# Optimization experiments

Measured on AMD Instinct MI355X. Metric: run time of the kernel, lower is better.

## Reference

```python
import jax, jax.numpy as jnp
import numpy as np

N, FIN, H, FOUT = 4096, 128, 4, 64
NEG_INF = -1e9


def _xavier(key, shape):
    fan_in, fan_out = shape[-2], shape[-1]
    limit = float(np.sqrt(6.0 / (fan_in + fan_out)))
    return jax.random.uniform(key, shape, jnp.float32, -limit, limit)


def setup_inputs() -> dict:
    key = jax.random.key(0)
    ks = jax.random.split(key, 7)
    x = jax.random.normal(ks[0], (N, FIN), jnp.float32)
    u = jax.random.uniform(ks[1], (N, N))
    mask = jnp.where(u < 0.02, 0.0, NEG_INF).astype(jnp.float32)
    idx = jnp.arange(N)
    mask = mask.at[idx, idx].set(0.0)
    proj_param = _xavier(ks[2], (H, FIN, FOUT))          # per-head projection
    score_src = _xavier(ks[3], (H, FOUT, 1))             # scoring_fn_source (IMP1 layout)
    score_tgt = _xavier(ks[4], (H, FOUT, 1))             # scoring_fn_target
    skip_w = _xavier(ks[5], (H * FOUT, FIN))             # skip_proj Linear weight
    bias = jnp.zeros((H * FOUT,), jnp.float32)
    return {"x": x, "mask": mask, "proj_param": proj_param,
            "score_src": score_src, "score_tgt": score_tgt,
            "skip_w": skip_w, "bias": bias}


def reference(x, mask, proj_param, score_src, score_tgt, skip_w, bias):
    # project: [1,N,Fin] @ [H,Fin,Fout] -> [H,N,Fout]
    h = jnp.einsum('nf,hfo->hno', x, proj_param)
    # additive (Bahdanau-style) scores
    s_src = jnp.matmul(h, score_src)                     # [H,N,1]
    s_tgt = jnp.matmul(h, score_tgt)                     # [H,N,1]
    all_scores = jax.nn.leaky_relu(s_src + jnp.swapaxes(s_tgt, 1, 2), 0.2)  # [H,N,N]
    attn = jax.nn.softmax(all_scores + mask[None, :, :], axis=-1)           # [H,N,N]
    # aggregate: [H,N,N] @ [H,N,Fout] -> [N,H,Fout]
    out = jnp.einsum('hnm,hmo->nho', attn, h)
    # skip connection (dims differ: Fin != H*Fout -> use skip_proj)
    out = out + jnp.matmul(x, skip_w.T).reshape(N, H, FOUT)
    out = out.reshape(N, H * FOUT) + bias                # concat heads + bias
    return jax.nn.elu(out)
```

## Files before the change

### kernel.cpp

```cpp
#include <hip/hip_runtime.h>
#include <hip/hip_bf16.h>
#include <math.h>


#define NN   4096
#define FIN  128
#define NH   4
#define FO   64
#define HF   256
#define SEG  96
#define LIST 192
#define GEMM_BLOCKS 512
#define SCAN_BLOCKS 1024
#define ROWS_PER    4

typedef unsigned short ushort_t;
typedef unsigned int uint4n __attribute__((ext_vector_type(4)));

__device__ __forceinline__ ushort_t f2bf(float f) {
    __hip_bfloat16 h = __float2bfloat16(f);
    union { __hip_bfloat16 h; ushort_t u; } c; c.h = h; return c.u;
}
__device__ __forceinline__ float bf2f(ushort_t u) {
    union { unsigned int i; float f; } c; c.i = ((unsigned int)u) << 16; return c.f;
}

__global__ __launch_bounds__(256) void k0_fused(
        const float* __restrict__ x,
        const float* __restrict__ proj,
        const float* __restrict__ skw,
        const float* __restrict__ asrc,
        const float* __restrict__ atgt,
        const unsigned int* __restrict__ mask,
        ushort_t* __restrict__ h2b, float* __restrict__ skip_ws,
        float* __restrict__ src4, float* __restrict__ tgt4,
        ushort_t* __restrict__ list, int* __restrict__ cnt) {
    __shared__ float sA[64 * 68];
    __shared__ float sB[64 * 64];
    const int tid = threadIdx.x;
    const int blk = blockIdx.x;

    if (blk >= GEMM_BLOCKS) {
        ushort_t* s_nbr = (ushort_t*)sA;
        int (*s_wt)[4]  = (int(*)[4])sB;
        const int lane = tid & 63, w = tid >> 6;
        const int row0 = (blk - GEMM_BLOCKS) * ROWS_PER;
        const uint4n* mb = (const uint4n*)mask;
        const size_t wl = (size_t)(w * 256 + lane);

        uint4n cur[4], nxt[4];
        #pragma unroll
        for (int s = 0; s < 4; s++)
            cur[s] = mb[(size_t)row0 * 1024 + wl + s * 64];

        for (int rr = 0; rr < ROWS_PER; rr++) {
            const int i = row0 + rr;
            if (rr + 1 < ROWS_PER) {
                #pragma unroll
                for (int s = 0; s < 4; s++)
                    nxt[s] = mb[(size_t)(i + 1) * 1024 + wl + s * 64];
            }
            int base = 0;
            #pragma unroll
            for (int s = 0; s < 4; s++) {
                #pragma unroll
                for (int e = 0; e < 4; e++) {
                    bool hit = (cur[s][e] & 0x7fffffffu) == 0u;
                    unsigned long long bal = __ballot(hit);
                    int pre = __builtin_amdgcn_mbcnt_hi(
                                  (unsigned int)(bal >> 32),
                                  __builtin_amdgcn_mbcnt_lo((unsigned int)bal, 0));
                    if (hit) {
                        int slot = base + pre;
                        if (slot < SEG)
                            s_nbr[w * SEG + slot] =
                                (ushort_t)(w * 1024 + s * 256 + lane * 4 + e);
                    }
                    base += (int)__popcll(bal);
                }
            }
            const int p = rr & 1;
            if (lane == 0) s_wt[p][w] = base < SEG ? base : SEG;
            __syncthreads();
            const int t0 = s_wt[p][0], t1 = s_wt[p][1],
                      t2 = s_wt[p][2], t3 = s_wt[p][3];
            const int off = (w > 0 ? t0 : 0) + (w > 1 ? t1 : 0) + (w > 2 ? t2 : 0);
            const int mine = s_wt[p][w];
            ushort_t* dst = list + (size_t)i * LIST;
            for (int kk = lane; kk < mine; kk += 64) {
                int pp = off + kk;
                if (pp < LIST) dst[pp] = s_nbr[w * SEG + kk];
            }
            if (tid == 0) {
                int tot = t0 + t1 + t2 + t3;
                cnt[i] = tot < LIST ? tot : LIST;
            }
            #pragma unroll
            for (int s = 0; s < 4; s++) cur[s] = nxt[s];
        }
        return;
    }

    const int bc = blk >> 6;
    const int i0 = (blk & 63) * 64;
    const int tx = tid & 15, ty = tid >> 4;
    const int r0 = ty << 2, c0 = tx << 2;
    float acc[4][4] = {};

    #pragma unroll
    for (int kb = 0; kb < FIN; kb += 64) {
        if (kb) __syncthreads();
        #pragma unroll
        for (int q = 0; q < 4; q++) {
            int s   = tid + q * 256;
            int row = s >> 4;
            int c4  = (s & 15) << 2;
            float4 v = *(const float4*)(x + (size_t)(i0 + row) * FIN + kb + c4);
            float* d = sA + row * 68 + c4;
            d[0] = v.x; d[1] = v.y; d[2] = v.z; d[3] = v.w;
        }
        if (bc < 4) {
            const float4* src = (const float4*)(proj + (size_t)bc * FIN * FO
                                                + (size_t)kb * FO);
            #pragma unroll
            for (int q = 0; q < 4; q++) {
                int s = tid + q * 256;
                *(float4*)(sB + (size_t)s * 4) = src[s];
            }
        } else {
            const float* sw = skw + (size_t)(bc - 4) * 64 * FIN;
            #pragma unroll
            for (int q = 0; q < 4; q++) {
                int s  = tid + q * 256;
                int c  = s & 63;
                int k4 = (s >> 6) << 2;
                float4 v = *(const float4*)(sw + (size_t)c * FIN + kb + k4);
                sB[(k4 + 0) * 64 + c] = v.x;
                sB[(k4 + 1) * 64 + c] = v.y;
                sB[(k4 + 2) * 64 + c] = v.z;
                sB[(k4 + 3) * 64 + c] = v.w;
            }
        }
        __syncthreads();

        #pragma unroll 2
        for (int k = 0; k < 64; k += 4) {
            alignas(16) float a[4][4];
            alignas(16) float b[4][4];
            #pragma unroll
            for (int rr = 0; rr < 4; rr++)
                *(float4*)a[rr] = *(const float4*)(sA + (r0 + rr) * 68 + k);
            #pragma unroll
            for (int kk = 0; kk < 4; kk++)
                *(float4*)b[kk] = *(const float4*)(sB + (k + kk) * 64 + c0);
            #pragma unroll
            for (int kk = 0; kk < 4; kk++)
                #pragma unroll
                for (int rr = 0; rr < 4; rr++)
                    #pragma unroll
                    for (int cc = 0; cc < 4; cc++)
                        acc[rr][cc] = fmaf(a[rr][kk], b[kk][cc], acc[rr][cc]);
        }
    }

    if (bc < 4) {
        #pragma unroll
        for (int rr = 0; rr < 4; rr++) {
            ushort4 hv;
            hv.x = f2bf(acc[rr][0]); hv.y = f2bf(acc[rr][1]);
            hv.z = f2bf(acc[rr][2]); hv.w = f2bf(acc[rr][3]);
            *(ushort4*)(h2b + (size_t)(i0 + r0 + rr) * HF + bc * 64 + c0) = hv;
        }
        float as[4], at[4];
        #pragma unroll
        for (int cc = 0; cc < 4; cc++) {
            as[cc] = asrc[bc * FO + c0 + cc];
            at[cc] = atgt[bc * FO + c0 + cc];
        }
        #pragma unroll
        for (int rr = 0; rr < 4; rr++) {
            float ps = acc[rr][0] * as[0] + acc[rr][1] * as[1]
                     + acc[rr][2] * as[2] + acc[rr][3] * as[3];
            float pt = acc[rr][0] * at[0] + acc[rr][1] * at[1]
                     + acc[rr][2] * at[2] + acc[rr][3] * at[3];
            #pragma unroll
            for (int off = 8; off >= 1; off >>= 1) {
                ps += __shfl_xor(ps, off, 64);
                pt += __shfl_xor(pt, off, 64);
            }
            if (tx == 0) {
                int i = i0 + r0 + rr;
                src4[(size_t)i * 4 + bc] = ps;
                tgt4[(size_t)i * 4 + bc] = pt;
            }
        }
    } else {
        float* dst = skip_ws + (size_t)i0 * HF + (bc - 4) * 64;
        #pragma unroll
        for (int rr = 0; rr < 4; rr++)
            *(float4*)(dst + (size_t)(r0 + rr) * HF + c0) = *(float4*)acc[rr];
    }
}

__global__ __launch_bounds__(256) void k2b_attn(
        const ushort_t* __restrict__ list,
        const int* __restrict__ cnt,
        const ushort_t* __restrict__ h2b,
        const float* __restrict__ skip_ws,
        const float* __restrict__ src4,
        const float* __restrict__ tgt4,
        const float* __restrict__ bias,
        float* __restrict__ out) {
    __shared__ float s_p[4][LIST];
    __shared__ int   s_j[LIST];
    const int tid  = threadIdx.x;
    const int lane = tid & 63, w = tid >> 6;
    const int i    = blockIdx.x;
    const int col  = w * 64 + lane;

    const float skipv = skip_ws[(size_t)i * HF + col];
    const float bv    = bias[col];
    const float sc    = src4[(size_t)i * 4 + w];
    int c = cnt[i];
    c = c < LIST ? c : LIST;

    const ushort_t* lp = list + (size_t)i * LIST;
    for (int kk = tid; kk < c; kk += 256) s_j[kk] = lp[kk];
    __syncthreads();

    float lsum = 0.f;
    for (int kk = lane; kk < c; kk += 64) {
        int j = s_j[kk];
        float p = sc + tgt4[(size_t)j * 4 + w];
        p = p > 0.f ? p : 0.2f * p;
        p = __expf(p);
        s_p[w][kk] = p;
        lsum += p;
    }
    #pragma unroll
    for (int off = 32; off >= 1; off >>= 1)
        lsum += __shfl_xor(lsum, off, 64);
    const float inv = lsum > 0.f ? 1.0f / lsum : 0.0f;

    const ushort_t* hp = h2b + col;
    const float* ps = s_p[w];
    float acc = 0.f;
    int kk = 0;
    for (; kk + 8 <= c; kk += 8) {
        int j0 = s_j[kk + 0], j1 = s_j[kk + 1], j2 = s_j[kk + 2], j3 = s_j[kk + 3];
        int j4 = s_j[kk + 4], j5 = s_j[kk + 5], j6 = s_j[kk + 6], j7 = s_j[kk + 7];
        float p0 = ps[kk + 0], p1 = ps[kk + 1], p2 = ps[kk + 2], p3 = ps[kk + 3];
        float p4 = ps[kk + 4], p5 = ps[kk + 5], p6 = ps[kk + 6], p7 = ps[kk + 7];
        float h0 = bf2f(hp[(size_t)j0 * HF]);
        float h1 = bf2f(hp[(size_t)j1 * HF]);
        float h2v = bf2f(hp[(size_t)j2 * HF]);
        float h3 = bf2f(hp[(size_t)j3 * HF]);
        float h4 = bf2f(hp[(size_t)j4 * HF]);
        float h5 = bf2f(hp[(size_t)j5 * HF]);
        float h6 = bf2f(hp[(size_t)j6 * HF]);
        float h7 = bf2f(hp[(size_t)j7 * HF]);
        acc = fmaf(p0, h0, acc);  acc = fmaf(p1, h1, acc);
        acc = fmaf(p2, h2v, acc); acc = fmaf(p3, h3, acc);
        acc = fmaf(p4, h4, acc);  acc = fmaf(p5, h5, acc);
        acc = fmaf(p6, h6, acc);  acc = fmaf(p7, h7, acc);
    }
    for (; kk < c; kk++)
        acc = fmaf(ps[kk], bf2f(hp[(size_t)s_j[kk] * HF]), acc);

    float vv = acc * inv + skipv + bv;
    vv = vv > 0.f ? vv : expm1f(vv);
    out[(size_t)i * HF + col] = vv;
}

extern "C" void kernel_launch(void* const* d_in, const int* in_sizes, int n_in,
                              void* d_out, int out_size, void* d_ws, size_t ws_size,
                              hipStream_t stream) {
    const float*        x    = (const float*)d_in[0];
    const unsigned int* mask = (const unsigned int*)d_in[1];
    const float*        proj = (const float*)d_in[2];
    const float*        asrc = (const float*)d_in[3];
    const float*        atgt = (const float*)d_in[4];
    const float*        skw  = (const float*)d_in[5];
    const float*        bias = (const float*)d_in[6];
    float*              out  = (float*)d_out;

    char* ws = (char*)d_ws;
    ushort_t* h2b     = (ushort_t*)ws;
    float*    skip_ws = (float*)(ws + (2u << 20));
    float*    src4    = (float*)(ws + (6u << 20));
    float*    tgt4    = (float*)(ws + (6u << 20) + (64u << 10));
    ushort_t* list    = (ushort_t*)(ws + (8u << 20));
    int*      cntp    = (int*)(ws + (10u << 20));

    hipLaunchKernelGGL(k0_fused, dim3(GEMM_BLOCKS + SCAN_BLOCKS), dim3(256),
                       0, stream,
                       x, proj, skw, asrc, atgt, mask,
                       h2b, skip_ws, src4, tgt4, list, cntp);
    hipLaunchKernelGGL(k2b_attn, dim3(NN), dim3(256), 0, stream,
                       list, cntp, h2b, skip_ws, src4, tgt4, bias, out);
}
```

Baseline: 135.9 us.

## Fuse mask scan into attention kernel and vectorize neighbor gather by row

The mask-to-neighbor-list compaction moves out of the GEMM kernel and into the attention kernel. Each block now scans its own mask row into shared memory, so the list and count no longer go through global memory. The aggregation now has each wave take every fourth neighbor and load a full 256-wide bf16 row as ushort4 per lane, with the four wave partials reduced through shared memory. The cost is that the mask read (64 MB) now sits on the attention kernel's critical path instead of overlapping with the GEMM blocks, plus extra syncs and shared-memory use per block.

New measurement: 127.1 us. 6.5% less time.

```diff
diff --git a/kernel.cpp b/kernel.cpp
--- a/kernel.cpp
+++ b/kernel.cpp
@@ -11,8 +11,6 @@
 #define SEG  96
 #define LIST 192
 #define GEMM_BLOCKS 512
-#define SCAN_BLOCKS 1024
-#define ROWS_PER    4
 
 typedef unsigned short ushort_t;
 typedef unsigned int uint4n __attribute__((ext_vector_type(4)));
@@ -25,81 +23,18 @@
     union { unsigned int i; float f; } c; c.i = ((unsigned int)u) << 16; return c.f;
 }
 
-__global__ __launch_bounds__(256) void k0_fused(
+__global__ __launch_bounds__(256) void k0_gemm(
         const float* __restrict__ x,
         const float* __restrict__ proj,
         const float* __restrict__ skw,
         const float* __restrict__ asrc,
         const float* __restrict__ atgt,
-        const unsigned int* __restrict__ mask,
         ushort_t* __restrict__ h2b, float* __restrict__ skip_ws,
-        float* __restrict__ src4, float* __restrict__ tgt4,
-        ushort_t* __restrict__ list, int* __restrict__ cnt) {
+        float* __restrict__ src4, float* __restrict__ tgt4) {
     __shared__ float sA[64 * 68];
     __shared__ float sB[64 * 64];
     const int tid = threadIdx.x;
     const int blk = blockIdx.x;
-
-    if (blk >= GEMM_BLOCKS) {
-        ushort_t* s_nbr = (ushort_t*)sA;
-        int (*s_wt)[4]  = (int(*)[4])sB;
-        const int lane = tid & 63, w = tid >> 6;
-        const int row0 = (blk - GEMM_BLOCKS) * ROWS_PER;
-        const uint4n* mb = (const uint4n*)mask;
-        const size_t wl = (size_t)(w * 256 + lane);
-
-        uint4n cur[4], nxt[4];
-        #pragma unroll
-        for (int s = 0; s < 4; s++)
-            cur[s] = mb[(size_t)row0 * 1024 + wl + s * 64];
-
-        for (int rr = 0; rr < ROWS_PER; rr++) {
-            const int i = row0 + rr;
-            if (rr + 1 < ROWS_PER) {
-                #pragma unroll
-                for (int s = 0; s < 4; s++)
-                    nxt[s] = mb[(size_t)(i + 1) * 1024 + wl + s * 64];
-            }
-            int base = 0;
-            #pragma unroll
-            for (int s = 0; s < 4; s++) {
-                #pragma unroll
-                for (int e = 0; e < 4; e++) {
-                    bool hit = (cur[s][e] & 0x7fffffffu) == 0u;
-                    unsigned long long bal = __ballot(hit);
-                    int pre = __builtin_amdgcn_mbcnt_hi(
-                                  (unsigned int)(bal >> 32),
-                                  __builtin_amdgcn_mbcnt_lo((unsigned int)bal, 0));
-                    if (hit) {
-                        int slot = base + pre;
-                        if (slot < SEG)
-                            s_nbr[w * SEG + slot] =
-                                (ushort_t)(w * 1024 + s * 256 + lane * 4 + e);
-                    }
-                    base += (int)__popcll(bal);
-                }
-            }
-            const int p = rr & 1;
-            if (lane == 0) s_wt[p][w] = base < SEG ? base : SEG;
-            __syncthreads();
-            const int t0 = s_wt[p][0], t1 = s_wt[p][1],
-                      t2 = s_wt[p][2], t3 = s_wt[p][3];
-            const int off = (w > 0 ? t0 : 0) + (w > 1 ? t1 : 0) + (w > 2 ? t2 : 0);
-            const int mine = s_wt[p][w];
-            ushort_t* dst = list + (size_t)i * LIST;
-            for (int kk = lane; kk < mine; kk += 64) {
-                int pp = off + kk;
-                if (pp < LIST) dst[pp] = s_nbr[w * SEG + kk];
-            }
-            if (tid == 0) {
-                int tot = t0 + t1 + t2 + t3;
-                cnt[i] = tot < LIST ? tot : LIST;
-            }
-            #pragma unroll
-            for (int s = 0; s < 4; s++) cur[s] = nxt[s];
-        }
-        return;
-    }
 
     const int bc = blk >> 6;
     const int i0 = (blk & 63) * 64;
@@ -202,30 +137,66 @@
     }
 }
 
-__global__ __launch_bounds__(256) void k2b_attn(
-        const ushort_t* __restrict__ list,
-        const int* __restrict__ cnt,
+__global__ __launch_bounds__(256) void k1_attn(
+        const unsigned int* __restrict__ mask,
         const ushort_t* __restrict__ h2b,
         const float* __restrict__ skip_ws,
         const float* __restrict__ src4,
         const float* __restrict__ tgt4,
         const float* __restrict__ bias,
         float* __restrict__ out) {
-    __shared__ float s_p[4][LIST];
-    __shared__ int   s_j[LIST];
+    __shared__ ushort_t s_seg[4][SEG];
+    __shared__ int      s_j[LIST];
+    __shared__ float    s_p[4][LIST + 1];
+    __shared__ float    s_red[4][256];
+    __shared__ int      s_cnt[4];
+    __shared__ float    s_inv[4];
+
     const int tid  = threadIdx.x;
     const int lane = tid & 63, w = tid >> 6;
     const int i    = blockIdx.x;
-    const int col  = w * 64 + lane;
-
-    const float skipv = skip_ws[(size_t)i * HF + col];
-    const float bv    = bias[col];
+
+    const uint4n* mb = (const uint4n*)mask + (size_t)i * 1024;
+    uint4n cur[4];
+    #pragma unroll
+    for (int s = 0; s < 4; s++)
+        cur[s] = mb[w * 256 + lane + s * 64];
+
+    const float skipv = skip_ws[(size_t)i * HF + tid];
+    const float bv    = bias[tid];
     const float sc    = src4[(size_t)i * 4 + w];
-    int c = cnt[i];
+
+    int base = 0;
+    #pragma unroll
+    for (int s = 0; s < 4; s++) {
+        #pragma unroll
+        for (int e = 0; e < 4; e++) {
+            bool hit = (cur[s][e] & 0x7fffffffu) == 0u;
+            unsigned long long bal = __ballot(hit);
+            int pre = __builtin_amdgcn_mbcnt_hi(
+                          (unsigned int)(bal >> 32),
+                          __builtin_amdgcn_mbcnt_lo((unsigned int)bal, 0));
+            if (hit) {
+                int slot = base + pre;
+                if (slot < SEG)
+                    s_seg[w][slot] =
+                        (ushort_t)(w * 1024 + s * 256 + lane * 4 + e);
+            }
+            base += (int)__popcll(bal);
+        }
+    }
+    if (lane == 0) s_cnt[w] = base < SEG ? base : SEG;
+    __syncthreads();
+
+    const int t0 = s_cnt[0], t1 = s_cnt[1], t2 = s_cnt[2], t3 = s_cnt[3];
+    const int off  = (w > 0 ? t0 : 0) + (w > 1 ? t1 : 0) + (w > 2 ? t2 : 0);
+    const int mine = s_cnt[w];
+    for (int kk = lane; kk < mine; kk += 64) {
+        int pp = off + kk;
+        if (pp < LIST) s_j[pp] = s_seg[w][kk];
+    }
+    int c = t0 + t1 + t2 + t3;
     c = c < LIST ? c : LIST;
-
-    const ushort_t* lp = list + (size_t)i * LIST;
-    for (int kk = tid; kk < c; kk += 256) s_j[kk] = lp[kk];
     __syncthreads();
 
     float lsum = 0.f;
@@ -238,38 +209,45 @@
         lsum += p;
     }
     #pragma unroll
-    for (int off = 32; off >= 1; off >>= 1)
-        lsum += __shfl_xor(lsum, off, 64);
-    const float inv = lsum > 0.f ? 1.0f / lsum : 0.0f;
-
-    const ushort_t* hp = h2b + col;
-    const float* ps = s_p[w];
-    float acc = 0.f;
-    int kk = 0;
-    for (; kk + 8 <= c; kk += 8) {
-        int j0 = s_j[kk + 0], j1 = s_j[kk + 1], j2 = s_j[kk + 2], j3 = s_j[kk + 3];
-        int j4 = s_j[kk + 4], j5 = s_j[kk + 5], j6 = s_j[kk + 6], j7 = s_j[kk + 7];
-        float p0 = ps[kk + 0], p1 = ps[kk + 1], p2 = ps[kk + 2], p3 = ps[kk + 3];
-        float p4 = ps[kk + 4], p5 = ps[kk + 5], p6 = ps[kk + 6], p7 = ps[kk + 7];
-        float h0 = bf2f(hp[(size_t)j0 * HF]);
-        float h1 = bf2f(hp[(size_t)j1 * HF]);
-        float h2v = bf2f(hp[(size_t)j2 * HF]);
-        float h3 = bf2f(hp[(size_t)j3 * HF]);
-        float h4 = bf2f(hp[(size_t)j4 * HF]);
-        float h5 = bf2f(hp[(size_t)j5 * HF]);
-        float h6 = bf2f(hp[(size_t)j6 * HF]);
-        float h7 = bf2f(hp[(size_t)j7 * HF]);
-        acc = fmaf(p0, h0, acc);  acc = fmaf(p1, h1, acc);
-        acc = fmaf(p2, h2v, acc); acc = fmaf(p3, h3, acc);
-        acc = fmaf(p4, h4, acc);  acc = fmaf(p5, h5, acc);
-        acc = fmaf(p6, h6, acc);  acc = fmaf(p7, h7, acc);
-    }
-    for (; kk < c; kk++)
-        acc = fmaf(ps[kk], bf2f(hp[(size_t)s_j[kk] * HF]), acc);
-
-    float vv = acc * inv + skipv + bv;
+    for (int o = 32; o >= 1; o >>= 1)
+        lsum += __shfl_xor(lsum, o, 64);
+    if (lane == 0) s_inv[w] = lsum > 0.f ? 1.0f / lsum : 0.0f;
+    __syncthreads();
+
+    const int h = lane >> 4;
+    const ushort_t* hp = h2b + 4 * lane;
+    float4 acc = {0.f, 0.f, 0.f, 0.f};
+    int kk = w;
+    for (; kk + 4 < c; kk += 8) {
+        int   j0 = s_j[kk],        j1 = s_j[kk + 4];
+        float p0 = s_p[h][kk],     p1 = s_p[h][kk + 4];
+        ushort4 a0 = *(const ushort4*)(hp + (size_t)j0 * HF);
+        ushort4 a1 = *(const ushort4*)(hp + (size_t)j1 * HF);
+        acc.x = fmaf(p0, bf2f(a0.x), acc.x);
+        acc.y = fmaf(p0, bf2f(a0.y), acc.y);
+        acc.z = fmaf(p0, bf2f(a0.z), acc.z);
+        acc.w = fmaf(p0, bf2f(a0.w), acc.w);
+        acc.x = fmaf(p1, bf2f(a1.x), acc.x);
+        acc.y = fmaf(p1, bf2f(a1.y), acc.y);
+        acc.z = fmaf(p1, bf2f(a1.z), acc.z);
+        acc.w = fmaf(p1, bf2f(a1.w), acc.w);
+    }
+    if (kk < c) {
+        int   j0 = s_j[kk];
+        float p0 = s_p[h][kk];
+        ushort4 a0 = *(const ushort4*)(hp + (size_t)j0 * HF);
+        acc.x = fmaf(p0, bf2f(a0.x), acc.x);
+        acc.y = fmaf(p0, bf2f(a0.y), acc.y);
+        acc.z = fmaf(p0, bf2f(a0.z), acc.z);
+        acc.w = fmaf(p0, bf2f(a0.w), acc.w);
+    }
+    *(float4*)&s_red[w][4 * lane] = acc;
+    __syncthreads();
+
+    float tot = s_red[0][tid] + s_red[1][tid] + s_red[2][tid] + s_red[3][tid];
+    float vv = tot * s_inv[tid >> 6] + skipv + bv;
     vv = vv > 0.f ? vv : expm1f(vv);
-    out[(size_t)i * HF + col] = vv;
+    out[(size_t)i * HF + tid] = vv;
 }
 
 extern "C" void kernel_launch(void* const* d_in, const int* in_sizes, int n_in,
@@ -289,13 +267,10 @@
     float*    skip_ws = (float*)(ws + (2u << 20));
     float*    src4    = (float*)(ws + (6u << 20));
     float*    tgt4    = (float*)(ws + (6u << 20) + (64u << 10));
-    ushort_t* list    = (ushort_t*)(ws + (8u << 20));
-    int*      cntp    = (int*)(ws + (10u << 20));
-
-    hipLaunchKernelGGL(k0_fused, dim3(GEMM_BLOCKS + SCAN_BLOCKS), dim3(256),
-                       0, stream,
-                       x, proj, skw, asrc, atgt, mask,
-                       h2b, skip_ws, src4, tgt4, list, cntp);
-    hipLaunchKernelGGL(k2b_attn, dim3(NN), dim3(256), 0, stream,
-                       list, cntp, h2b, skip_ws, src4, tgt4, bias, out);
-}
+
+    hipLaunchKernelGGL(k0_gemm, dim3(GEMM_BLOCKS), dim3(256), 0, stream,
+                       x, proj, skw, asrc, atgt,
+                       h2b, skip_ws, src4, tgt4);
+    hipLaunchKernelGGL(k1_attn, dim3(NN), dim3(256), 0, stream,
+                       mask, h2b, skip_ws, src4, tgt4, bias, out);
+}
```
